# Performance work log

Hardware: AMD Instinct MI355X
Metric: run time of the kernel (lower is better)

Reference implementation:

```python
import jax, jax.numpy as jnp
import numpy as np
from jax import lax

B, CIN, CH, HW, K = 256, 256, 256, 16, 3


def setup_inputs() -> dict:
    key = jax.random.key(0)
    ks = jax.random.split(key, 9)
    s = 0.05
    return {
        "x": jax.random.normal(ks[0], (B, CIN, HW, HW), dtype=jnp.float32),
        "h": jax.random.normal(ks[1], (B, CH, HW, HW), dtype=jnp.float32),
        "c": jax.random.normal(ks[2], (B, CH, HW, HW), dtype=jnp.float32),
        # stacked x-branch conv weights for gates [i, f, c, o]; no bias (matches torch code)
        "Wx": jax.random.normal(ks[3], (4 * CH, CIN, K, K), dtype=jnp.float32) * s,
        # stacked h-branch conv weights for gates [i, f, c, o]; with bias
        "Wh": jax.random.normal(ks[4], (4 * CH, CH, K, K), dtype=jnp.float32) * s,
        "bh": jax.random.normal(ks[5], (4 * CH,), dtype=jnp.float32) * s,
        # peephole params (torch inits them to zeros; use small randn to exercise the math)
        "Wci": jax.random.normal(ks[6], (1, CH, HW, HW), dtype=jnp.float32) * s,
        "Wcf": jax.random.normal(ks[7], (1, CH, HW, HW), dtype=jnp.float32) * s,
        "Wco": jax.random.normal(ks[8], (1, CH, HW, HW), dtype=jnp.float32) * s,
    }


def _conv(x, w):
    # same-padding 2D conv, NCHW/OIHW
    return lax.conv_general_dilated(
        x, w, window_strides=(1, 1), padding="SAME",
        dimension_numbers=("NCHW", "OIHW", "NCHW"))


def reference(x, h, c, Wx, Wh, bh, Wci, Wcf, Wco):
    gx = _conv(x, Wx)                                   # [B, 4*CH, H, W]
    gh = _conv(h, Wh) + bh[None, :, None, None]         # [B, 4*CH, H, W]
    xi, xf, xc, xo = jnp.split(gx, 4, axis=1)
    hi, hf, hc, ho = jnp.split(gh, 4, axis=1)
    i_t = jax.nn.sigmoid(xi + hi + Wci * c)
    f_t = jax.nn.sigmoid(xf + hf + Wcf * c)
    c_t = f_t * c + i_t * jnp.tanh(xc + hc)
    o_t = jax.nn.sigmoid(xo + ho + Wco * c_t)
    h_t = o_t * jnp.tanh(c_t)
    return (h_t, c_t)
```

## Files before the change

### kernel.cpp

```cpp
#include <hip/hip_runtime.h>


typedef __bf16 bf16x8 __attribute__((ext_vector_type(8)));
typedef float f32x16 __attribute__((ext_vector_type(16)));

#define PLANE_B  20736u
#define XH_BYTES (4096u * PLANE_B)
#define OUT_HALF 16777216u

__device__ inline void gload_lds16(const void* g, void* l) {
    __builtin_amdgcn_global_load_lds(
        (const __attribute__((address_space(1))) void*)g,
        (__attribute__((address_space(3))) void*)l, 16, 0, 0);
}

__global__ __launch_bounds__(256) void xh_transform(
    const float* __restrict__ x, const float* __restrict__ hh,
    unsigned char* __restrict__ xh)
{
    int blk = blockIdx.x;
    int b = blk >> 4, ibk = blk & 15;
    const float* src = (ibk < 8) ? (x  + ((size_t)(b*256 + ibk*32)) * 256)
                                 : (hh + ((size_t)(b*256 + (ibk-8)*32)) * 256);
    int t = threadIdx.x;
    uint32_t w[16];
#pragma unroll
    for (int i = 0; i < 16; ++i) {
        __bf16 lo = (__bf16)src[(size_t)(2*i  )*256 + t];
        __bf16 hi = (__bf16)src[(size_t)(2*i+1)*256 + t];
        w[i] = (uint32_t)__builtin_bit_cast(unsigned short, lo)
             | ((uint32_t)__builtin_bit_cast(unsigned short, hi) << 16);
    }
    unsigned char* plane = xh + (size_t)blk * PLANE_B;
    int p = ((t >> 4) + 1)*18 + (t & 15) + 1;
    uint32_t key  = (uint32_t)(p & 7) << 4;
    uint32_t base = (uint32_t)p * 64u;
#pragma unroll
    for (int k = 0; k < 4; ++k)
        *(uint4*)(plane + ((base + 16u*k) ^ key)) =
            uint4{w[4*k], w[4*k+1], w[4*k+2], w[4*k+3]};
    if (t < 68) {
        int pb;
        if      (t < 18) pb = t;
        else if (t < 36) pb = 17*18 + (t - 18);
        else if (t < 52) pb = (t - 35)*18;
        else             pb = (t - 51)*18 + 17;
        uint32_t kb = (uint32_t)(pb & 7) << 4;
        uint32_t bb = (uint32_t)pb * 64u;
        uint4 z{0u,0u,0u,0u};
#pragma unroll
        for (int k = 0; k < 4; ++k)
            *(uint4*)(plane + ((bb + 16u*k) ^ kb)) = z;
    }
}

__global__ __launch_bounds__(256) void w_transform(
    const float* __restrict__ Wx, const float* __restrict__ Wh,
    __bf16* __restrict__ Wt)
{
    int idx  = blockIdx.x * 256 + threadIdx.x;
    int lane = idx & 63;
    int chunk = idx >> 6;
    int f     = chunk & 1;
    int half  = (chunk >> 1) & 1;
    int pos   = (chunk >> 2) % 9;
    int rest  = (chunk >> 2) / 9;
    int ibk   = rest & 15;
    int cbnh  = rest >> 4;
    int nh = cbnh & 1, cb = cbnh >> 1;
    int row = lane & 31, hl = lane >> 5;
    int gate = row & 3, ch8 = row >> 2;
    int oc  = gate*256 + cb*32 + (nh*2 + f)*8 + ch8;
    int ic0 = ibk*32 + half*16 + hl*8;
    bf16x8 v;
#pragma unroll
    for (int j = 0; j < 8; ++j) {
        int ic = ic0 + j;
        float w = (ic < 256) ? Wx[((size_t)oc*256 + ic      )*9 + pos]
                             : Wh[((size_t)oc*256 + (ic-256))*9 + pos];
        v[j] = (__bf16)w;
    }
    *(bf16x8*)(Wt + (size_t)chunk*512 + (size_t)lane*8) = v;
}

__global__ __launch_bounds__(256, 2) void convlstm_main(
    const unsigned char* __restrict__ xh, const __bf16* __restrict__ Wt,
    const float* __restrict__ bh,  const float* __restrict__ cin,
    const float* __restrict__ Wci, const float* __restrict__ Wcf,
    const float* __restrict__ Wco, float* __restrict__ out)
{
    int bid = blockIdx.x;
    int cb  = bid & 7;
    int nh  = (bid >> 3) & 1;
    int b   = bid >> 4;
    int tid = threadIdx.x;
    int lane = tid & 63, wv = tid >> 6;
    int l31 = lane & 31, hl = lane >> 5;

    __shared__ __align__(16) unsigned char lds[2][24576];

    f32x16 acc[2][2];
#pragma unroll
    for (int f = 0; f < 2; ++f) {
        int fg = nh*2 + f;
        f32x16 v;
#pragma unroll
        for (int r = 0; r < 16; ++r) {
            int gate = r & 3, q = r >> 2;
            v[r] = bh[gate*256 + cb*32 + fg*8 + 2*q + hl];
        }
        acc[0][f] = v; acc[1][f] = v;
    }

    const unsigned char* planes = xh + (size_t)b * (16u * PLANE_B);

#pragma unroll
    for (int k = 0; k < 6; ++k)
        gload_lds16(planes + (size_t)(wv*6 + k)*1024u + (size_t)lane*16u,
                    &lds[0][(wv*6 + k)*1024 + lane*16]);

    int m0 = wv*64 + l31, m1 = m0 + 32;
    int pb0 = (m0 >> 4)*18 + (m0 & 15);
    int pb1 = (m1 >> 4)*18 + (m1 & 15);
    const uint32_t kbase = (uint32_t)(hl*16);
    uint32_t baddr[9][2];
#pragma unroll
    for (int pos = 0; pos < 9; ++pos) {
        int d = (pos/3)*18 + (pos%3);
        int p0 = pb0 + d, p1 = pb1 + d;
        baddr[pos][0] = ((uint32_t)p0*64u + kbase) ^ (((uint32_t)(p0 & 7)) << 4);
        baddr[pos][1] = ((uint32_t)p1*64u + kbase) ^ (((uint32_t)(p1 & 7)) << 4);
    }
    const char* lds0 = (const char*)&lds[0][0];

    const __bf16* abase = Wt + (size_t)(cb*2 + nh)*294912u + (size_t)lane*8;

    bf16x8 A[3][2];
    A[0][0] = *(const bf16x8*)(abase + 0);
    A[0][1] = *(const bf16x8*)(abase + 512);
    A[1][0] = *(const bf16x8*)(abase + 1024);
    A[1][1] = *(const bf16x8*)(abase + 1536);

    __syncthreads();

#define IBK_PHASES(LAST)                                                     \
    {                                                                        \
        bf16x8 Bb[2][2];                                                     \
        Bb[0][0] = *(const bf16x8*)(lds0 + baddr[0][0]);                     \
        Bb[0][1] = *(const bf16x8*)(lds0 + baddr[0][1]);                     \
        _Pragma("unroll")                                                    \
        for (int p = 0; p < 18; ++p) {                                       \
              \
            {                                                                \
                const int tp = p + 2;                                        \
                const int xo = (tp < 18) ? 0 : ((LAST) ? -18432 : 0);        \
                const int off = ((tp < 18)                                   \
                    ? ((tp>>1)*2048 + (tp&1)*1024)                           \
                    : (18432 + (((tp-18)>>1)*2048 + ((tp-18)&1)*1024))) + xo;\
                A[(p+2)%3][0] = *(const bf16x8*)(abase + off);               \
                A[(p+2)%3][1] = *(const bf16x8*)(abase + off + 512);         \
            }                                                                \
            if (p == 1 && !(LAST)) {                                         \
                const unsigned char* np_ = planes + (size_t)(ibk+1)*PLANE_B; \
                _Pragma("unroll")                                            \
                for (int k = 0; k < 6; ++k)                                  \
                    gload_lds16(np_ + (size_t)(wv*6 + k)*1024u               \
                                    + (size_t)lane*16u,                      \
                                &lds[(ibk & 1) ^ 1][(wv*6 + k)*1024          \
                                                    + lane*16]);             \
            }                                                                \
            if (p < 17) {                                                    \
                const int np = p + 1;                                        \
                uint32_t a0 = baddr[np>>1][0] ^ (uint32_t)((np&1)*32);       \
                uint32_t a1 = baddr[np>>1][1] ^ (uint32_t)((np&1)*32);       \
                Bb[np&1][0] = *(const bf16x8*)(lds0 + a0);                   \
                Bb[np&1][1] = *(const bf16x8*)(lds0 + a1);                   \
            }                                                                \
            __builtin_amdgcn_s_setprio(1);                                   \
            acc[0][0] = __builtin_amdgcn_mfma_f32_32x32x16_bf16(A[p%3][0], Bb[p&1][0], acc[0][0], 0, 0, 0); \
            acc[0][1] = __builtin_amdgcn_mfma_f32_32x32x16_bf16(A[p%3][1], Bb[p&1][0], acc[0][1], 0, 0, 0); \
            acc[1][0] = __builtin_amdgcn_mfma_f32_32x32x16_bf16(A[p%3][0], Bb[p&1][1], acc[1][0], 0, 0, 0); \
            acc[1][1] = __builtin_amdgcn_mfma_f32_32x32x16_bf16(A[p%3][1], Bb[p&1][1], acc[1][1], 0, 0, 0); \
            __builtin_amdgcn_s_setprio(0);                                   \
        }                                                                    \
    }

    int flipd = 24576;
    for (int ibk = 0; ibk < 15; ++ibk) {
        IBK_PHASES(0)
#pragma unroll
        for (int pos = 0; pos < 9; ++pos) {
            baddr[pos][0] += (uint32_t)flipd;
            baddr[pos][1] += (uint32_t)flipd;
        }
        flipd = -flipd;
        abase += 18432;
        asm volatile("s_waitcnt vmcnt(4) lgkmcnt(0)" ::: "memory");
        __builtin_amdgcn_s_barrier();
        __builtin_amdgcn_sched_barrier(0);
    }
    {
        const int ibk = 15;
        (void)ibk;
        IBK_PHASES(1)
    }
#undef IBK_PHASES

    float* outh = out;
    float* outc = out + (size_t)OUT_HALF;
    const size_t bOff = (size_t)b * (256*256);
#pragma unroll
    for (int mf = 0; mf < 2; ++mf) {
        int m = wv*64 + mf*32 + l31;
#pragma unroll
        for (int f = 0; f < 2; ++f) {
            int fg = nh*2 + f;
#pragma unroll
            for (int q = 0; q < 4; ++q) {
                int ch = cb*32 + fg*8 + 2*q + hl;
                size_t pidx = (size_t)ch*256 + (size_t)m;
                size_t idx  = bOff + pidx;
                float cv = cin[idx];
                float pi = acc[mf][f][4*q+0];
                float pf = acc[mf][f][4*q+1];
                float pc = acc[mf][f][4*q+2];
                float po = acc[mf][f][4*q+3];
                float it = 1.f/(1.f + __expf(-(pi + Wci[pidx]*cv)));
                float ft = 1.f/(1.f + __expf(-(pf + Wcf[pidx]*cv)));
                float tc = 1.f - 2.f/(1.f + __expf(2.f*pc));
                float ct = ft*cv + it*tc;
                float ot = 1.f/(1.f + __expf(-(po + Wco[pidx]*ct)));
                float th = 1.f - 2.f/(1.f + __expf(2.f*ct));
                outh[idx] = ot*th;
                outc[idx] = ct;
            }
        }
    }
}

extern "C" void kernel_launch(void* const* d_in, const int* in_sizes, int n_in,
                              void* d_out, int out_size, void* d_ws, size_t ws_size,
                              hipStream_t stream)
{
    const float* x   = (const float*)d_in[0];
    const float* h   = (const float*)d_in[1];
    const float* c   = (const float*)d_in[2];
    const float* Wx  = (const float*)d_in[3];
    const float* Wh  = (const float*)d_in[4];
    const float* bh  = (const float*)d_in[5];
    const float* Wci = (const float*)d_in[6];
    const float* Wcf = (const float*)d_in[7];
    const float* Wco = (const float*)d_in[8];
    float* out = (float*)d_out;

    unsigned char* xh = (unsigned char*)d_ws;
    __bf16* Wt = (__bf16*)(xh + (size_t)XH_BYTES + 4096);

    hipLaunchKernelGGL(xh_transform, dim3(4096), dim3(256), 0, stream, x, h, xh);
    hipLaunchKernelGGL(w_transform,  dim3(2304), dim3(256), 0, stream, Wx, Wh, Wt);
    hipLaunchKernelGGL(convlstm_main, dim3(4096), dim3(256), 0, stream,
                       xh, Wt, bh, c, Wci, Wcf, Wco, out);
}
```

Baseline: 630.9 us.

## Merge channel halves into one block with 2x2 wave tiling for reuse

Each block now covers all 32 channels for its channel block (four filter groups) instead of splitting them across two blocks by nh. Waves are arranged as 2 (pixel) x 2 (filter) with each wave computing 128 pixels x 2 filter groups, which doubles the MFMA work per LDS and weight load. The grid is halved and the weight layout is re-indexed to match. Input planes are staged into LDS half as often in total, at the cost of more accumulator registers (8 f32x16 tiles per wave), which may pressure occupancy under launch_bounds(256,2).

```diff
diff --git a/kernel.cpp b/kernel.cpp
--- a/kernel.cpp
+++ b/kernel.cpp
@@ -61,16 +61,15 @@
     int idx  = blockIdx.x * 256 + threadIdx.x;
     int lane = idx & 63;
     int chunk = idx >> 6;
-    int f     = chunk & 1;
-    int half  = (chunk >> 1) & 1;
-    int pos   = (chunk >> 2) % 9;
-    int rest  = (chunk >> 2) / 9;
-    int ibk   = rest & 15;
-    int cbnh  = rest >> 4;
-    int nh = cbnh & 1, cb = cbnh >> 1;
+    int f    = chunk & 3;
+    int half = (chunk >> 2) & 1;
+    int pos  = (chunk >> 3) % 9;
+    int rest = (chunk >> 3) / 9;
+    int ibk  = rest & 15;
+    int cb   = rest >> 4;
     int row = lane & 31, hl = lane >> 5;
     int gate = row & 3, ch8 = row >> 2;
-    int oc  = gate*256 + cb*32 + (nh*2 + f)*8 + ch8;
+    int oc  = gate*256 + cb*32 + f*8 + ch8;
     int ic0 = ibk*32 + half*16 + hl*8;
     bf16x8 v;
 #pragma unroll
@@ -84,32 +83,32 @@
 }
 
 __global__ __launch_bounds__(256, 2) void convlstm_main(
-    const unsigned char* __restrict__ xh, const __bf16* __restrict__ Wt,
+    const unsigned char* __restrict__ xh, const unsigned char* __restrict__ Wtb,
     const float* __restrict__ bh,  const float* __restrict__ cin,
     const float* __restrict__ Wci, const float* __restrict__ Wcf,
     const float* __restrict__ Wco, float* __restrict__ out)
 {
     int bid = blockIdx.x;
     int cb  = bid & 7;
-    int nh  = (bid >> 3) & 1;
-    int b   = bid >> 4;
+    int b   = bid >> 3;
     int tid = threadIdx.x;
     int lane = tid & 63, wv = tid >> 6;
+    int wm = wv & 1, wf = wv >> 1;
     int l31 = lane & 31, hl = lane >> 5;
 
     __shared__ __align__(16) unsigned char lds[2][24576];
 
-    f32x16 acc[2][2];
-#pragma unroll
-    for (int f = 0; f < 2; ++f) {
-        int fg = nh*2 + f;
+    f32x16 acc[4][2];
+#pragma unroll
+    for (int j = 0; j < 2; ++j) {
+        int fg = wf*2 + j;
         f32x16 v;
 #pragma unroll
         for (int r = 0; r < 16; ++r) {
             int gate = r & 3, q = r >> 2;
             v[r] = bh[gate*256 + cb*32 + fg*8 + 2*q + hl];
         }
-        acc[0][f] = v; acc[1][f] = v;
+        acc[0][j] = v; acc[1][j] = v; acc[2][j] = v; acc[3][j] = v;
     }
 
     const unsigned char* planes = xh + (size_t)b * (16u * PLANE_B);
@@ -119,46 +118,44 @@
         gload_lds16(planes + (size_t)(wv*6 + k)*1024u + (size_t)lane*16u,
                     &lds[0][(wv*6 + k)*1024 + lane*16]);
 
-    int m0 = wv*64 + l31, m1 = m0 + 32;
+    int m0 = wm*128 + l31;
     int pb0 = (m0 >> 4)*18 + (m0 & 15);
-    int pb1 = (m1 >> 4)*18 + (m1 & 15);
     const uint32_t kbase = (uint32_t)(hl*16);
     uint32_t baddr[9][2];
 #pragma unroll
     for (int pos = 0; pos < 9; ++pos) {
         int d = (pos/3)*18 + (pos%3);
-        int p0 = pb0 + d, p1 = pb1 + d;
-        baddr[pos][0] = ((uint32_t)p0*64u + kbase) ^ (((uint32_t)(p0 & 7)) << 4);
-        baddr[pos][1] = ((uint32_t)p1*64u + kbase) ^ (((uint32_t)(p1 & 7)) << 4);
+        int pp = pb0 + d;
+        uint32_t a = ((uint32_t)pp*64u + kbase) ^ (((uint32_t)(pp & 7)) << 4);
+        baddr[pos][0] = a;
+        baddr[pos][1] = (a + 2304u) ^ 64u;
     }
     const char* lds0 = (const char*)&lds[0][0];
 
-    const __bf16* abase = Wt + (size_t)(cb*2 + nh)*294912u + (size_t)lane*8;
-
-    bf16x8 A[3][2];
-    A[0][0] = *(const bf16x8*)(abase + 0);
-    A[0][1] = *(const bf16x8*)(abase + 512);
-    A[1][0] = *(const bf16x8*)(abase + 1024);
-    A[1][1] = *(const bf16x8*)(abase + 1536);
+    const unsigned char* aptr = Wtb + (size_t)cb*1179648u
+                                    + (size_t)(wf*2048) + (size_t)(lane*16);
+
+    bf16x8 A[2][2], Bb[2][4];
+    A[0][0] = *(const bf16x8*)(aptr + 0);
+    A[0][1] = *(const bf16x8*)(aptr + 1024);
 
     __syncthreads();
 
 #define IBK_PHASES(LAST)                                                     \
     {                                                                        \
-        bf16x8 Bb[2][2];                                                     \
+           \
         Bb[0][0] = *(const bf16x8*)(lds0 + baddr[0][0]);                     \
         Bb[0][1] = *(const bf16x8*)(lds0 + baddr[0][1]);                     \
+        Bb[0][2] = *(const bf16x8*)(lds0 + baddr[0][0] + 4608);              \
+        Bb[0][3] = *(const bf16x8*)(lds0 + baddr[0][1] + 4608);              \
         _Pragma("unroll")                                                    \
         for (int p = 0; p < 18; ++p) {                                       \
-              \
+                                \
             {                                                                \
-                const int tp = p + 2;                                        \
-                const int xo = (tp < 18) ? 0 : ((LAST) ? -18432 : 0);        \
-                const int off = ((tp < 18)                                   \
-                    ? ((tp>>1)*2048 + (tp&1)*1024)                           \
-                    : (18432 + (((tp-18)>>1)*2048 + ((tp-18)&1)*1024))) + xo;\
-                A[(p+2)%3][0] = *(const bf16x8*)(abase + off);               \
-                A[(p+2)%3][1] = *(const bf16x8*)(abase + off + 512);         \
+                const int noff = ((LAST) && p == 17) ? (17*4096)             \
+                                                     : ((p+1)*4096);         \
+                A[(p+1)&1][0] = *(const bf16x8*)(aptr + noff);               \
+                A[(p+1)&1][1] = *(const bf16x8*)(aptr + noff + 1024);        \
             }                                                                \
             if (p == 1 && !(LAST)) {                                         \
                 const unsigned char* np_ = planes + (size_t)(ibk+1)*PLANE_B; \
@@ -169,18 +166,26 @@
                                 &lds[(ibk & 1) ^ 1][(wv*6 + k)*1024          \
                                                     + lane*16]);             \
             }                                                                \
+                                \
             if (p < 17) {                                                    \
                 const int np = p + 1;                                        \
-                uint32_t a0 = baddr[np>>1][0] ^ (uint32_t)((np&1)*32);       \
-                uint32_t a1 = baddr[np>>1][1] ^ (uint32_t)((np&1)*32);       \
+                const uint32_t hx = (uint32_t)((np & 1)*32);                 \
+                uint32_t a0 = baddr[np>>1][0] ^ hx;                          \
+                uint32_t a1 = baddr[np>>1][1] ^ hx;                          \
                 Bb[np&1][0] = *(const bf16x8*)(lds0 + a0);                   \
                 Bb[np&1][1] = *(const bf16x8*)(lds0 + a1);                   \
+                Bb[np&1][2] = *(const bf16x8*)(lds0 + a0 + 4608);            \
+                Bb[np&1][3] = *(const bf16x8*)(lds0 + a1 + 4608);            \
             }                                                                \
             __builtin_amdgcn_s_setprio(1);                                   \
-            acc[0][0] = __builtin_amdgcn_mfma_f32_32x32x16_bf16(A[p%3][0], Bb[p&1][0], acc[0][0], 0, 0, 0); \
-            acc[0][1] = __builtin_amdgcn_mfma_f32_32x32x16_bf16(A[p%3][1], Bb[p&1][0], acc[0][1], 0, 0, 0); \
-            acc[1][0] = __builtin_amdgcn_mfma_f32_32x32x16_bf16(A[p%3][0], Bb[p&1][1], acc[1][0], 0, 0, 0); \
-            acc[1][1] = __builtin_amdgcn_mfma_f32_32x32x16_bf16(A[p%3][1], Bb[p&1][1], acc[1][1], 0, 0, 0); \
+            acc[0][0] = __builtin_amdgcn_mfma_f32_32x32x16_bf16(A[p&1][0], Bb[p&1][0], acc[0][0], 0, 0, 0); \
+            acc[0][1] = __builtin_amdgcn_mfma_f32_32x32x16_bf16(A[p&1][1], Bb[p&1][0], acc[0][1], 0, 0, 0); \
+            acc[1][0] = __builtin_amdgcn_mfma_f32_32x32x16_bf16(A[p&1][0], Bb[p&1][1], acc[1][0], 0, 0, 0); \
+            acc[1][1] = __builtin_amdgcn_mfma_f32_32x32x16_bf16(A[p&1][1], Bb[p&1][1], acc[1][1], 0, 0, 0); \
+            acc[2][0] = __builtin_amdgcn_mfma_f32_32x32x16_bf16(A[p&1][0], Bb[p&1][2], acc[2][0], 0, 0, 0); \
+            acc[2][1] = __builtin_amdgcn_mfma_f32_32x32x16_bf16(A[p&1][1], Bb[p&1][2], acc[2][1], 0, 0, 0); \
+            acc[3][0] = __builtin_amdgcn_mfma_f32_32x32x16_bf16(A[p&1][0], Bb[p&1][3], acc[3][0], 0, 0, 0); \
+            acc[3][1] = __builtin_amdgcn_mfma_f32_32x32x16_bf16(A[p&1][1], Bb[p&1][3], acc[3][1], 0, 0, 0); \
             __builtin_amdgcn_s_setprio(0);                                   \
         }                                                                    \
     }
@@ -194,8 +199,8 @@
             baddr[pos][1] += (uint32_t)flipd;
         }
         flipd = -flipd;
-        abase += 18432;
-        asm volatile("s_waitcnt vmcnt(4) lgkmcnt(0)" ::: "memory");
+        aptr += 73728;
+        asm volatile("s_waitcnt vmcnt(2) lgkmcnt(0)" ::: "memory");
         __builtin_amdgcn_s_barrier();
         __builtin_amdgcn_sched_barrier(0);
     }
@@ -210,21 +215,21 @@
     float* outc = out + (size_t)OUT_HALF;
     const size_t bOff = (size_t)b * (256*256);
 #pragma unroll
-    for (int mf = 0; mf < 2; ++mf) {
-        int m = wv*64 + mf*32 + l31;
-#pragma unroll
-        for (int f = 0; f < 2; ++f) {
-            int fg = nh*2 + f;
+    for (int mf = 0; mf < 4; ++mf) {
+        int m = wm*128 + mf*32 + l31;
+#pragma unroll
+        for (int j = 0; j < 2; ++j) {
+            int fg = wf*2 + j;
 #pragma unroll
             for (int q = 0; q < 4; ++q) {
                 int ch = cb*32 + fg*8 + 2*q + hl;
                 size_t pidx = (size_t)ch*256 + (size_t)m;
                 size_t idx  = bOff + pidx;
                 float cv = cin[idx];
-                float pi = acc[mf][f][4*q+0];
-                float pf = acc[mf][f][4*q+1];
-                float pc = acc[mf][f][4*q+2];
-                float po = acc[mf][f][4*q+3];
+                float pi = acc[mf][j][4*q+0];
+                float pf = acc[mf][j][4*q+1];
+                float pc = acc[mf][j][4*q+2];
+                float po = acc[mf][j][4*q+3];
                 float it = 1.f/(1.f + __expf(-(pi + Wci[pidx]*cv)));
                 float ft = 1.f/(1.f + __expf(-(pf + Wcf[pidx]*cv)));
                 float tc = 1.f - 2.f/(1.f + __expf(2.f*pc));
@@ -254,10 +259,11 @@
     float* out = (float*)d_out;
 
     unsigned char* xh = (unsigned char*)d_ws;
-    __bf16* Wt = (__bf16*)(xh + (size_t)XH_BYTES + 4096);
+    unsigned char* wtb = xh + (size_t)XH_BYTES + 4096;
 
     hipLaunchKernelGGL(xh_transform, dim3(4096), dim3(256), 0, stream, x, h, xh);
-    hipLaunchKernelGGL(w_transform,  dim3(2304), dim3(256), 0, stream, Wx, Wh, Wt);
-    hipLaunchKernelGGL(convlstm_main, dim3(4096), dim3(256), 0, stream,
-                       xh, Wt, bh, c, Wci, Wcf, Wco, out);
-}
+    hipLaunchKernelGGL(w_transform,  dim3(2304), dim3(256), 0, stream,
+                       Wx, Wh, (__bf16*)wtb);
+    hipLaunchKernelGGL(convlstm_main, dim3(2048), dim3(256), 0, stream,
+                       xh, wtb, bh, c, Wci, Wcf, Wco, out);
+}
```

After: 588.0 us. 1.07x faster.
